# Performance work log

Hardware: AMD Instinct MI355X
Metric: run time of the kernel (lower is better)

Reference implementation:

```python
import jax, jax.numpy as jnp
import numpy as np

E = 20    # number of residue types (rc.restypes)
NB = 2    # num_blocks per AngleHead
NA = 7    # num_angles
C_S = 384
C_H = 128
BS, L = 8, 2048


def setup_inputs() -> dict:
    key = jax.random.key(0)
    ks = jax.random.split(key, 16)
    sc = 0.02
    return {
        "s": jax.random.normal(ks[0], (BS, L, C_S), dtype=jnp.float32),
        "s_init": jax.random.normal(ks[1], (BS, L, C_S), dtype=jnp.float32),
        "aatype": jax.random.randint(ks[2], (BS, L), 0, E, dtype=jnp.int32),
        # stacked per-residue-type AngleHead params
        "Win": jax.random.normal(ks[3], (E, C_S, C_H), dtype=jnp.float32) * sc,
        "b_in": jax.random.normal(ks[4], (E, C_H), dtype=jnp.float32) * sc,
        "Winit": jax.random.normal(ks[5], (E, C_S, C_H), dtype=jnp.float32) * sc,
        "b_init2": jax.random.normal(ks[6], (E, C_H), dtype=jnp.float32) * sc,
        "Wb1": jax.random.normal(ks[7], (E, NB, C_H, C_H), dtype=jnp.float32) * sc,
        "bb1": jax.random.normal(ks[8], (E, NB, C_H), dtype=jnp.float32) * sc,
        "Wb2": jax.random.normal(ks[9], (E, NB, C_H, C_H), dtype=jnp.float32) * sc,
        "bb2": jax.random.normal(ks[10], (E, NB, C_H), dtype=jnp.float32) * sc,
        "Wout": jax.random.normal(ks[11], (E, C_H, NA * 2), dtype=jnp.float32) * sc,
        "b_out": jax.random.normal(ks[12], (E, NA * 2), dtype=jnp.float32) * sc,
    }


def reference(s, s_init, aatype, Win, b_in, Winit, b_init2, Wb1, bb1, Wb2, bb2, Wout, b_out):
    relu = jax.nn.relu
    bs, seq_len, c_s = s.shape
    N = bs * seq_len
    sf = s.reshape(N, c_s)          # [N, c_s]
    si = s_init.reshape(N, c_s)     # [N, c_s]

    # Dense dispatch: run every token through all E per-type heads, then
    # combine with the one-hot routing mask (math identical to the torch
    # gather/scatter loop over residue types).
    h = jnp.einsum('nd,edh->neh', relu(sf), Win) + b_in            # [N,E,H]
    h = h + jnp.einsum('nd,edh->neh', relu(si), Winit) + b_init2   # [N,E,H]

    for b in range(NB):  # ResidualBlock1d: s + W2 @ relu(W1 @ relu(s))
        a = jnp.einsum('neh,ehk->nek', relu(h), Wb1[:, b]) + bb1[:, b]
        a = jnp.einsum('nek,ekh->neh', relu(a), Wb2[:, b]) + bb2[:, b]
        h = h + a

    out = jnp.einsum('neh,eho->neo', relu(h), Wout) + b_out        # [N,E,2*NA]
    sel = jax.nn.one_hot(aatype.reshape(N), E, dtype=out.dtype)    # [N,E]
    ang = jnp.einsum('neo,ne->no', out, sel).reshape(bs, seq_len, NA, 2)

    # F.normalize(dim=-1): x / max(||x||, eps)
    nrm = jnp.maximum(jnp.linalg.norm(ang, axis=-1, keepdims=True), 1e-12)
    return ang / nrm
```

## Files before the change

### kernel.cpp

```cpp
#include <hip/hip_runtime.h>
#include <math.h>

#define E_TYPES 20
#define NBLK 2
#define NANG 7
#define CS 384
#define CH 128
#define N_TOK (8 * 2048)
#define TOK 32
#define TPB 256
#define KC 128
#define MAX_TILES (N_TOK / TOK + E_TYPES)
#define PADN 2048

#define CNT_OFF 0
#define PERM_OFF 64
#define WT1_OFF (256 * 1024)
#define WT1_SZ  (20 * 8 * 24 * 2048)
#define WTR_OFF (WT1_OFF + WT1_SZ)

typedef __attribute__((ext_vector_type(8))) short bfrag;
typedef __attribute__((ext_vector_type(4))) float f32x4;

__device__ __forceinline__ void split_bf16(float x, unsigned short& h, unsigned short& l) {
    unsigned int u = __float_as_uint(x);
    unsigned int hb = (u + 0x7FFFu + ((u >> 16) & 1u)) & 0xFFFF0000u;
    h = (unsigned short)(hb >> 16);
    float r = x - __uint_as_float(hb);
    unsigned int v = __float_as_uint(r);
    l = (unsigned short)((v + 0x7FFFu + ((v >> 16) & 1u)) >> 16);
}

__global__ __launch_bounds__(TPB)
void prep_k(const float* __restrict__ Win, const float* __restrict__ Winit,
            const float* __restrict__ Wb1, const float* __restrict__ Wb2,
            const int* __restrict__ aatype, int* __restrict__ wsI,
            unsigned short* __restrict__ wt)
{
    __shared__ unsigned short tp[4][2][32][134];
    __shared__ int lh[E_TYPES], lcur[E_TYPES];
    int bid = blockIdx.x, t = threadIdx.x;

    if (bid < 64) {
        if (t < E_TYPES) { lh[t] = 0; lcur[t] = 0; }
        __syncthreads();
        for (int i = t; i < bid * 256; i += 256) atomicAdd(&lh[aatype[i]], 1);
        __syncthreads();
        int idx = bid * 256 + t;
        int e = aatype[idx];
        int r = lh[e] + atomicAdd(&lcur[e], 1);
        if (r < PADN) wsI[PERM_OFF + e * PADN + r] = idx;
        if (bid == 63) {
            __syncthreads();
            if (t < E_TYPES) wsI[CNT_OFF + t] = lh[t] + lcur[t];
        }
        return;
    }

    int w = t >> 6, lane = t & 63, lane15 = lane & 15, quad = lane >> 4;
    int wid = (bid - 64) * 4 + w;
    const float* srcbase;
    int phase1, e, kt, m4 = 0;
    if (wid < 480) {
        phase1 = 1;
        e = wid / 24; kt = wid % 24;
        srcbase = (kt < 12) ? Win   + ((size_t)e * CS + kt * 32) * CH
                            : Winit + ((size_t)e * CS + (kt - 12) * 32) * CH;
    } else {
        phase1 = 0;
        int rid = wid - 480;
        e = rid >> 4; m4 = (rid >> 2) & 3; kt = rid & 3;
        const float* W = (m4 & 1) ? Wb2 : Wb1;
        srcbase = W + (((size_t)e * NBLK + (m4 >> 1)) * CH + kt * 32) * CH;
    }

    #pragma unroll 4
    for (int i = 0; i < 16; i++) {
        int idx = i * 64 + lane;
        int row = idx >> 5, c4 = idx & 31;
        float4 v = *(const float4*)(srcbase + (size_t)row * CH + c4 * 4);
        ushort4 hv, lv;
        split_bf16(v.x, hv.x, lv.x);
        split_bf16(v.y, hv.y, lv.y);
        split_bf16(v.z, hv.z, lv.z);
        split_bf16(v.w, hv.w, lv.w);
        *(ushort4*)&tp[w][0][row][c4 * 4] = hv;
        *(ushort4*)&tp[w][1][row][c4 * 4] = lv;
    }
    #pragma unroll
    for (int nt = 0; nt < 8; nt++) {
        bfrag hb, lb;
        #pragma unroll
        for (int j = 0; j < 8; j++) {
            hb[j] = (short)tp[w][0][quad * 8 + j][nt * 16 + lane15];
            lb[j] = (short)tp[w][1][quad * 8 + j][nt * 16 + lane15];
        }
        size_t blk = phase1 ? (size_t)((e * 8 + nt) * 24 + kt)
                            : (size_t)((((e * 4 + m4) * 8) + nt) * 4 + kt);
        unsigned short* dst = wt + (phase1 ? WT1_OFF / 2 : WTR_OFF / 2)
                              + blk * 1024 + lane * 8;
        *(bfrag*)dst = hb;
        *(bfrag*)(dst + 512) = lb;
    }
}

#define MFMA(a, b, c) __builtin_amdgcn_mfma_f32_16x16x32_bf16((a), (b), (c), 0, 0, 0)

__global__ __launch_bounds__(TPB)
void angle_main(const float* __restrict__ s, const float* __restrict__ si,
                const float* __restrict__ b_in, const float* __restrict__ b_init2,
                const float* __restrict__ bb1, const float* __restrict__ bb2,
                const float* __restrict__ Wout, const float* __restrict__ b_out,
                const int* __restrict__ wsI, const unsigned short* __restrict__ wt,
                float* __restrict__ out)
{
    __shared__ __align__(16) unsigned short Afrag[2][2][512][8];
    __shared__ float Hf[TOK][132];
    __shared__ float Of[TOK][16];
    __shared__ int ptok[TOK];
    __shared__ int poffs[E_TYPES + 1];

    int t = threadIdx.x;
    if (t == 0) {
        int off = 0;
        for (int e = 0; e < E_TYPES; e++) {
            poffs[e] = off;
            off += (wsI[CNT_OFF + e] + TOK - 1) & ~(TOK - 1);
        }
        poffs[E_TYPES] = off;
    }
    __syncthreads();

    int pos = blockIdx.x * TOK;
    if (pos >= poffs[E_TYPES]) return;
    int e = 0;
    while (e < E_TYPES - 1 && pos >= poffs[e + 1]) e++;
    int n = wsI[CNT_OFF + e] - (pos - poffs[e]);
    if (n > TOK) n = TOK;
    if (t < TOK)
        ptok[t] = wsI[PERM_OFF + e * PADN + (pos - poffs[e]) + ((t < n) ? t : 0)];
    __syncthreads();

    int w = t >> 6, lane = t & 63, lane15 = lane & 15, quad = lane >> 4;
    int nc0 = (2 * w) * 16 + lane15, nc1 = nc0 + 16;

    const bfrag* wt1 = (const bfrag*)((const char*)wt + WT1_OFF);
    const bfrag* wtr = (const bfrag*)((const char*)wt + WTR_OFF);

    f32x4 acc[2][2];
    {
        float bv0 = b_in[e * CH + nc0] + b_init2[e * CH + nc0];
        float bv1 = b_in[e * CH + nc1] + b_init2[e * CH + nc1];
        #pragma unroll
        for (int mt = 0; mt < 2; mt++) {
            acc[mt][0] = (f32x4){bv0, bv0, bv0, bv0};
            acc[mt][1] = (f32x4){bv1, bv1, bv1, bv1};
        }
    }

    int stok = t >> 3, sc = t & 7;
    const float* rowp_s  = s  + (size_t)ptok[stok] * CS;
    const float* rowp_si = si + (size_t)ptok[stok] * CS;

    float4 pf[2][4];
    #pragma unroll
    for (int q = 0; q < 4; q++)
        pf[0][q] = *(const float4*)(rowp_s + sc * 4 + 32 * q);

    #pragma unroll
    for (int c = 0; c < 6; c++) {
        int buf = c & 1;
        __syncthreads();
        #pragma unroll
        for (int q = 0; q < 4; q++) {
            float4 v = pf[buf][q];
            ushort4 hv, lv;
            split_bf16(fmaxf(v.x, 0.f), hv.x, lv.x);
            split_bf16(fmaxf(v.y, 0.f), hv.y, lv.y);
            split_bf16(fmaxf(v.z, 0.f), hv.z, lv.z);
            split_bf16(fmaxf(v.w, 0.f), hv.w, lv.w);
            int fi = (q * 4 + (sc >> 1)) * 32 + stok;
            *(ushort4*)&Afrag[buf][0][fi][(sc & 1) * 4] = hv;
            *(ushort4*)&Afrag[buf][1][fi][(sc & 1) * 4] = lv;
        }
        if (c + 1 < 6) {
            const float* rp = ((c + 1) < 3 ? rowp_s : rowp_si) + ((c + 1) % 3) * KC;
            #pragma unroll
            for (int q = 0; q < 4; q++)
                pf[(c + 1) & 1][q] = *(const float4*)(rp + sc * 4 + 32 * q);
        }
        __syncthreads();
        #pragma unroll
        for (int ks = 0; ks < 4; ks++) {
            int kb = c * 4 + ks;
            int fib = (ks * 4 + quad) * 32;
            bfrag ah0 = *(const bfrag*)&Afrag[buf][0][fib + lane15][0];
            bfrag ah1 = *(const bfrag*)&Afrag[buf][0][fib + 16 + lane15][0];
            bfrag al0 = *(const bfrag*)&Afrag[buf][1][fib + lane15][0];
            bfrag al1 = *(const bfrag*)&Afrag[buf][1][fib + 16 + lane15][0];
            size_t b0 = ((size_t)(e * 8 + 2 * w) * 24 + kb) * 128;
            size_t b1 = ((size_t)(e * 8 + 2 * w + 1) * 24 + kb) * 128;
            bfrag bh0 = wt1[b0 + lane], bl0 = wt1[b0 + 64 + lane];
            bfrag bh1 = wt1[b1 + lane], bl1 = wt1[b1 + 64 + lane];
            acc[0][0] = MFMA(ah0, bh0, acc[0][0]);
            acc[0][0] = MFMA(ah0, bl0, acc[0][0]);
            acc[0][0] = MFMA(al0, bh0, acc[0][0]);
            acc[0][1] = MFMA(ah0, bh1, acc[0][1]);
            acc[0][1] = MFMA(ah0, bl1, acc[0][1]);
            acc[0][1] = MFMA(al0, bh1, acc[0][1]);
            acc[1][0] = MFMA(ah1, bh0, acc[1][0]);
            acc[1][0] = MFMA(ah1, bl0, acc[1][0]);
            acc[1][0] = MFMA(al1, bh0, acc[1][0]);
            acc[1][1] = MFMA(ah1, bh1, acc[1][1]);
            acc[1][1] = MFMA(ah1, bl1, acc[1][1]);
            acc[1][1] = MFMA(al1, bh1, acc[1][1]);
        }
    }

    #pragma unroll
    for (int b = 0; b < NBLK; b++) {
        f32x4 a2[2][2];
        #pragma unroll
        for (int stage = 0; stage < 2; stage++) {
            int g = 2 * b + stage;
            __syncthreads();
            #pragma unroll
            for (int mt = 0; mt < 2; mt++)
                #pragma unroll
                for (int nl = 0; nl < 2; nl++) {
                    f32x4 v = (stage == 0) ? acc[mt][nl] : a2[mt][nl];
                    int nn = (2 * w + nl) * 16 + lane15;
                    int fib = ((nn >> 5) * 4 + ((nn >> 3) & 3)) * 32;
                    int j = nn & 7;
                    #pragma unroll
                    for (int r = 0; r < 4; r++) {
                        int m = mt * 16 + quad * 4 + r;
                        unsigned short hh, ll;
                        split_bf16(fmaxf(v[r], 0.f), hh, ll);
                        Afrag[0][0][fib + m][j] = hh;
                        Afrag[0][1][fib + m][j] = ll;
                    }
                }
            __syncthreads();

            const float* bias = (stage == 0) ? bb1 : bb2;
            f32x4 an[2][2];
            {
                float bv0 = bias[(e * NBLK + b) * CH + nc0];
                float bv1 = bias[(e * NBLK + b) * CH + nc1];
                #pragma unroll
                for (int mt = 0; mt < 2; mt++) {
                    an[mt][0] = (f32x4){bv0, bv0, bv0, bv0};
                    an[mt][1] = (f32x4){bv1, bv1, bv1, bv1};
                }
            }
            #pragma unroll
            for (int ks = 0; ks < 4; ks++) {
                int fib = (ks * 4 + quad) * 32;
                bfrag ah0 = *(const bfrag*)&Afrag[0][0][fib + lane15][0];
                bfrag ah1 = *(const bfrag*)&Afrag[0][0][fib + 16 + lane15][0];
                bfrag al0 = *(const bfrag*)&Afrag[0][1][fib + lane15][0];
                bfrag al1 = *(const bfrag*)&Afrag[0][1][fib + 16 + lane15][0];
                size_t b0 = ((size_t)((e * 4 + g) * 8 + 2 * w) * 4 + ks) * 128;
                size_t b1 = ((size_t)((e * 4 + g) * 8 + 2 * w + 1) * 4 + ks) * 128;
                bfrag bh0 = wtr[b0 + lane], bl0 = wtr[b0 + 64 + lane];
                bfrag bh1 = wtr[b1 + lane], bl1 = wtr[b1 + 64 + lane];
                an[0][0] = MFMA(ah0, bh0, an[0][0]);
                an[0][0] = MFMA(ah0, bl0, an[0][0]);
                an[0][0] = MFMA(al0, bh0, an[0][0]);
                an[0][1] = MFMA(ah0, bh1, an[0][1]);
                an[0][1] = MFMA(ah0, bl1, an[0][1]);
                an[0][1] = MFMA(al0, bh1, an[0][1]);
                an[1][0] = MFMA(ah1, bh0, an[1][0]);
                an[1][0] = MFMA(ah1, bl0, an[1][0]);
                an[1][0] = MFMA(al1, bh0, an[1][0]);
                an[1][1] = MFMA(ah1, bh1, an[1][1]);
                an[1][1] = MFMA(ah1, bl1, an[1][1]);
                an[1][1] = MFMA(al1, bh1, an[1][1]);
            }
            if (stage == 0) {
                #pragma unroll
                for (int mt = 0; mt < 2; mt++)
                    #pragma unroll
                    for (int nl = 0; nl < 2; nl++) a2[mt][nl] = an[mt][nl];
            } else {
                #pragma unroll
                for (int mt = 0; mt < 2; mt++)
                    #pragma unroll
                    for (int nl = 0; nl < 2; nl++) acc[mt][nl] += an[mt][nl];
            }
        }
    }

    __syncthreads();
    #pragma unroll
    for (int mt = 0; mt < 2; mt++)
        #pragma unroll
        for (int nl = 0; nl < 2; nl++) {
            f32x4 v = acc[mt][nl];
            int nn = (2 * w + nl) * 16 + lane15;
            #pragma unroll
            for (int r = 0; r < 4; r++)
                Hf[mt * 16 + quad * 4 + r][nn] = fmaxf(v[r], 0.f);
        }
    __syncthreads();

    const float* WoutE = Wout + (size_t)e * CH * (NANG * 2);
    const float* boutE = b_out + (size_t)e * (NANG * 2);
    for (int idx = t; idx < n * (NANG * 2); idx += TPB) {
        int i = idx / (NANG * 2);
        int o = idx % (NANG * 2);
        float v = boutE[o];
        #pragma unroll 4
        for (int k = 0; k < CH; k++)
            v = fmaf(Hf[i][k], WoutE[(size_t)k * (NANG * 2) + o], v);
        Of[i][o] = v;
    }
    __syncthreads();

    for (int idx = t; idx < n * NANG; idx += TPB) {
        int i = idx / NANG;
        int a = idx % NANG;
        float x = Of[i][2 * a];
        float y = Of[i][2 * a + 1];
        float nr = fmaxf(sqrtf(x * x + y * y), 1e-12f);
        size_t base = (size_t)ptok[i] * (NANG * 2) + 2 * a;
        out[base]     = x / nr;
        out[base + 1] = y / nr;
    }
}

extern "C" void kernel_launch(void* const* d_in, const int* in_sizes, int n_in,
                              void* d_out, int out_size, void* d_ws, size_t ws_size,
                              hipStream_t stream) {
    const float* s       = (const float*)d_in[0];
    const float* s_init  = (const float*)d_in[1];
    const int*   aatype  = (const int*)d_in[2];
    const float* Win     = (const float*)d_in[3];
    const float* b_in    = (const float*)d_in[4];
    const float* Winit   = (const float*)d_in[5];
    const float* b_init2 = (const float*)d_in[6];
    const float* Wb1     = (const float*)d_in[7];
    const float* bb1     = (const float*)d_in[8];
    const float* Wb2     = (const float*)d_in[9];
    const float* bb2     = (const float*)d_in[10];
    const float* Wout    = (const float*)d_in[11];
    const float* b_out   = (const float*)d_in[12];
    int* wsI = (int*)d_ws;
    unsigned short* wt = (unsigned short*)d_ws;
    float* out = (float*)d_out;

    hipLaunchKernelGGL(prep_k, dim3(64 + 200), dim3(TPB), 0, stream,
                       Win, Winit, Wb1, Wb2, aatype, wsI, wt);
    hipLaunchKernelGGL(angle_main, dim3(MAX_TILES), dim3(TPB), 0, stream,
                       s, s_init, b_in, b_init2, bb1, bb2, Wout, b_out,
                       wsI, wt, out);
}
```

Before: 164.8 us.

## Split token tile across 8 waves, alias shared memory, remap block order

```diff
diff --git a/kernel.cpp b/kernel.cpp
--- a/kernel.cpp
+++ b/kernel.cpp
@@ -8,9 +8,10 @@
 #define CH 128
 #define N_TOK (8 * 2048)
 #define TOK 32
-#define TPB 256
-#define KC 128
+#define TPB 512
+#define PREPB 256
 #define MAX_TILES (N_TOK / TOK + E_TYPES)
+#define GRID_M 536
 #define PADN 2048
 
 #define CNT_OFF 0
@@ -31,7 +32,7 @@
     l = (unsigned short)((v + 0x7FFFu + ((v >> 16) & 1u)) >> 16);
 }
 
-__global__ __launch_bounds__(TPB)
+__global__ __launch_bounds__(PREPB)
 void prep_k(const float* __restrict__ Win, const float* __restrict__ Winit,
             const float* __restrict__ Wb1, const float* __restrict__ Wb2,
             const int* __restrict__ aatype, int* __restrict__ wsI,
@@ -114,9 +115,11 @@
                 const int* __restrict__ wsI, const unsigned short* __restrict__ wt,
                 float* __restrict__ out)
 {
-    __shared__ __align__(16) unsigned short Afrag[2][2][512][8];
-    __shared__ float Hf[TOK][132];
-    __shared__ float Of[TOK][16];
+    __shared__ __align__(16) unsigned char smem_raw[32768];
+    typedef unsigned short AfragT[2][2][512][8];
+    AfragT& Afrag = *reinterpret_cast<AfragT*>(smem_raw);
+    float (*Hf)[130] = reinterpret_cast<float(*)[130]>(smem_raw);
+    float (*Of)[16]  = reinterpret_cast<float(*)[16]>(smem_raw + 16640);
     __shared__ int ptok[TOK];
     __shared__ int poffs[E_TYPES + 1];
 
@@ -131,7 +134,9 @@
     }
     __syncthreads();
 
-    int pos = blockIdx.x * TOK;
+    int bid = blockIdx.x;
+    int tile = (bid & 7) * (GRID_M / 8) + (bid >> 3);
+    int pos = tile * TOK;
     if (pos >= poffs[E_TYPES]) return;
     int e = 0;
     while (e < E_TYPES - 1 && pos >= poffs[e + 1]) e++;
@@ -139,170 +144,141 @@
     if (n > TOK) n = TOK;
     if (t < TOK)
         ptok[t] = wsI[PERM_OFF + e * PADN + (pos - poffs[e]) + ((t < n) ? t : 0)];
-    __syncthreads();
 
     int w = t >> 6, lane = t & 63, lane15 = lane & 15, quad = lane >> 4;
-    int nc0 = (2 * w) * 16 + lane15, nc1 = nc0 + 16;
+    int mw = w >> 2;
+    int np = w & 3;
+    int nc0 = (2 * np) * 16 + lane15, nc1 = nc0 + 16;
+
+    __syncthreads();
 
     const bfrag* wt1 = (const bfrag*)((const char*)wt + WT1_OFF);
     const bfrag* wtr = (const bfrag*)((const char*)wt + WTR_OFF);
 
-    f32x4 acc[2][2];
+    f32x4 acc[2];
     {
         float bv0 = b_in[e * CH + nc0] + b_init2[e * CH + nc0];
         float bv1 = b_in[e * CH + nc1] + b_init2[e * CH + nc1];
-        #pragma unroll
-        for (int mt = 0; mt < 2; mt++) {
-            acc[mt][0] = (f32x4){bv0, bv0, bv0, bv0};
-            acc[mt][1] = (f32x4){bv1, bv1, bv1, bv1};
-        }
-    }
-
-    int stok = t >> 3, sc = t & 7;
+        acc[0] = (f32x4){bv0, bv0, bv0, bv0};
+        acc[1] = (f32x4){bv1, bv1, bv1, bv1};
+    }
+
+    int stok = t >> 4, sc = t & 15;
     const float* rowp_s  = s  + (size_t)ptok[stok] * CS;
     const float* rowp_si = si + (size_t)ptok[stok] * CS;
 
-    float4 pf[2][4];
-    #pragma unroll
-    for (int q = 0; q < 4; q++)
-        pf[0][q] = *(const float4*)(rowp_s + sc * 4 + 32 * q);
+    float4 pf[2][2];
+    #pragma unroll
+    for (int q = 0; q < 2; q++)
+        pf[0][q] = *(const float4*)(rowp_s + sc * 4 + 64 * q);
 
     #pragma unroll
     for (int c = 0; c < 6; c++) {
         int buf = c & 1;
         __syncthreads();
         #pragma unroll
-        for (int q = 0; q < 4; q++) {
+        for (int q = 0; q < 2; q++) {
             float4 v = pf[buf][q];
             ushort4 hv, lv;
             split_bf16(fmaxf(v.x, 0.f), hv.x, lv.x);
             split_bf16(fmaxf(v.y, 0.f), hv.y, lv.y);
             split_bf16(fmaxf(v.z, 0.f), hv.z, lv.z);
             split_bf16(fmaxf(v.w, 0.f), hv.w, lv.w);
-            int fi = (q * 4 + (sc >> 1)) * 32 + stok;
+            int fi = ((sc >> 1) + 8 * q) * 32 + stok;
             *(ushort4*)&Afrag[buf][0][fi][(sc & 1) * 4] = hv;
             *(ushort4*)&Afrag[buf][1][fi][(sc & 1) * 4] = lv;
         }
         if (c + 1 < 6) {
-            const float* rp = ((c + 1) < 3 ? rowp_s : rowp_si) + ((c + 1) % 3) * KC;
+            const float* rp = ((c + 1) < 3 ? rowp_s : rowp_si) + ((c + 1) % 3) * 128;
             #pragma unroll
-            for (int q = 0; q < 4; q++)
-                pf[(c + 1) & 1][q] = *(const float4*)(rp + sc * 4 + 32 * q);
+            for (int q = 0; q < 2; q++)
+                pf[(c + 1) & 1][q] = *(const float4*)(rp + sc * 4 + 64 * q);
         }
         __syncthreads();
         #pragma unroll
         for (int ks = 0; ks < 4; ks++) {
             int kb = c * 4 + ks;
-            int fib = (ks * 4 + quad) * 32;
-            bfrag ah0 = *(const bfrag*)&Afrag[buf][0][fib + lane15][0];
-            bfrag ah1 = *(const bfrag*)&Afrag[buf][0][fib + 16 + lane15][0];
-            bfrag al0 = *(const bfrag*)&Afrag[buf][1][fib + lane15][0];
-            bfrag al1 = *(const bfrag*)&Afrag[buf][1][fib + 16 + lane15][0];
-            size_t b0 = ((size_t)(e * 8 + 2 * w) * 24 + kb) * 128;
-            size_t b1 = ((size_t)(e * 8 + 2 * w + 1) * 24 + kb) * 128;
+            int fib = (ks * 4 + quad) * 32 + mw * 16;
+            bfrag ah = *(const bfrag*)&Afrag[buf][0][fib + lane15][0];
+            bfrag al = *(const bfrag*)&Afrag[buf][1][fib + lane15][0];
+            size_t b0 = ((size_t)(e * 8 + 2 * np) * 24 + kb) * 128;
+            size_t b1 = ((size_t)(e * 8 + 2 * np + 1) * 24 + kb) * 128;
             bfrag bh0 = wt1[b0 + lane], bl0 = wt1[b0 + 64 + lane];
             bfrag bh1 = wt1[b1 + lane], bl1 = wt1[b1 + 64 + lane];
-            acc[0][0] = MFMA(ah0, bh0, acc[0][0]);
-            acc[0][0] = MFMA(ah0, bl0, acc[0][0]);
-            acc[0][0] = MFMA(al0, bh0, acc[0][0]);
-            acc[0][1] = MFMA(ah0, bh1, acc[0][1]);
-            acc[0][1] = MFMA(ah0, bl1, acc[0][1]);
-            acc[0][1] = MFMA(al0, bh1, acc[0][1]);
-            acc[1][0] = MFMA(ah1, bh0, acc[1][0]);
-            acc[1][0] = MFMA(ah1, bl0, acc[1][0]);
-            acc[1][0] = MFMA(al1, bh0, acc[1][0]);
-            acc[1][1] = MFMA(ah1, bh1, acc[1][1]);
-            acc[1][1] = MFMA(ah1, bl1, acc[1][1]);
-            acc[1][1] = MFMA(al1, bh1, acc[1][1]);
-        }
-    }
-
+            acc[0] = MFMA(ah, bh0, acc[0]);
+            acc[0] = MFMA(ah, bl0, acc[0]);
+            acc[0] = MFMA(al, bh0, acc[0]);
+            acc[1] = MFMA(ah, bh1, acc[1]);
+            acc[1] = MFMA(ah, bl1, acc[1]);
+            acc[1] = MFMA(al, bh1, acc[1]);
+        }
+    }
+
+    f32x4 a2[2];
     #pragma unroll
     for (int b = 0; b < NBLK; b++) {
-        f32x4 a2[2][2];
         #pragma unroll
         for (int stage = 0; stage < 2; stage++) {
             int g = 2 * b + stage;
             __syncthreads();
             #pragma unroll
-            for (int mt = 0; mt < 2; mt++)
+            for (int nl = 0; nl < 2; nl++) {
+                f32x4 v = (stage == 0) ? acc[nl] : a2[nl];
+                int nn = (2 * np + nl) * 16 + lane15;
+                int fib = ((nn >> 5) * 4 + ((nn >> 3) & 3)) * 32;
+                int j = nn & 7;
                 #pragma unroll
-                for (int nl = 0; nl < 2; nl++) {
-                    f32x4 v = (stage == 0) ? acc[mt][nl] : a2[mt][nl];
-                    int nn = (2 * w + nl) * 16 + lane15;
-                    int fib = ((nn >> 5) * 4 + ((nn >> 3) & 3)) * 32;
-                    int j = nn & 7;
-                    #pragma unroll
-                    for (int r = 0; r < 4; r++) {
-                        int m = mt * 16 + quad * 4 + r;
-                        unsigned short hh, ll;
-                        split_bf16(fmaxf(v[r], 0.f), hh, ll);
-                        Afrag[0][0][fib + m][j] = hh;
-                        Afrag[0][1][fib + m][j] = ll;
-                    }
+                for (int r = 0; r < 4; r++) {
+                    int m = mw * 16 + quad * 4 + r;
+                    unsigned short hh, ll;
+                    split_bf16(fmaxf(v[r], 0.f), hh, ll);
+                    Afrag[0][0][fib + m][j] = hh;
+                    Afrag[0][1][fib + m][j] = ll;
                 }
+            }
             __syncthreads();
 
             const float* bias = (stage == 0) ? bb1 : bb2;
-            f32x4 an[2][2];
+            f32x4 an[2];
             {
                 float bv0 = bias[(e * NBLK + b) * CH + nc0];
                 float bv1 = bias[(e * NBLK + b) * CH + nc1];
-                #pragma unroll
-                for (int mt = 0; mt < 2; mt++) {
-                    an[mt][0] = (f32x4){bv0, bv0, bv0, bv0};
-                    an[mt][1] = (f32x4){bv1, bv1, bv1, bv1};
-                }
+                an[0] = (f32x4){bv0, bv0, bv0, bv0};
+                an[1] = (f32x4){bv1, bv1, bv1, bv1};
             }
             #pragma unroll
             for (int ks = 0; ks < 4; ks++) {
-                int fib = (ks * 4 + quad) * 32;
-                bfrag ah0 = *(const bfrag*)&Afrag[0][0][fib + lane15][0];
-                bfrag ah1 = *(const bfrag*)&Afrag[0][0][fib + 16 + lane15][0];
-                bfrag al0 = *(const bfrag*)&Afrag[0][1][fib + lane15][0];
-                bfrag al1 = *(const bfrag*)&Afrag[0][1][fib + 16 + lane15][0];
-                size_t b0 = ((size_t)((e * 4 + g) * 8 + 2 * w) * 4 + ks) * 128;
-                size_t b1 = ((size_t)((e * 4 + g) * 8 + 2 * w + 1) * 4 + ks) * 128;
+                int fib = (ks * 4 + quad) * 32 + mw * 16;
+                bfrag ah = *(const bfrag*)&Afrag[0][0][fib + lane15][0];
+                bfrag al = *(const bfrag*)&Afrag[0][1][fib + lane15][0];
+                size_t b0 = ((size_t)((e * 4 + g) * 8 + 2 * np) * 4 + ks) * 128;
+                size_t b1 = ((size_t)((e * 4 + g) * 8 + 2 * np + 1) * 4 + ks) * 128;
                 bfrag bh0 = wtr[b0 + lane], bl0 = wtr[b0 + 64 + lane];
                 bfrag bh1 = wtr[b1 + lane], bl1 = wtr[b1 + 64 + lane];
-                an[0][0] = MFMA(ah0, bh0, an[0][0]);
-                an[0][0] = MFMA(ah0, bl0, an[0][0]);
-                an[0][0] = MFMA(al0, bh0, an[0][0]);
-                an[0][1] = MFMA(ah0, bh1, an[0][1]);
-                an[0][1] = MFMA(ah0, bl1, an[0][1]);
-                an[0][1] = MFMA(al0, bh1, an[0][1]);
-                an[1][0] = MFMA(ah1, bh0, an[1][0]);
-                an[1][0] = MFMA(ah1, bl0, an[1][0]);
-                an[1][0] = MFMA(al1, bh0, an[1][0]);
-                an[1][1] = MFMA(ah1, bh1, an[1][1]);
-                an[1][1] = MFMA(ah1, bl1, an[1][1]);
-                an[1][1] = MFMA(al1, bh1, an[1][1]);
+                an[0] = MFMA(ah, bh0, an[0]);
+                an[0] = MFMA(ah, bl0, an[0]);
+                an[0] = MFMA(al, bh0, an[0]);
+                an[1] = MFMA(ah, bh1, an[1]);
+                an[1] = MFMA(ah, bl1, an[1]);
+                an[1] = MFMA(al, bh1, an[1]);
             }
             if (stage == 0) {
-                #pragma unroll
-                for (int mt = 0; mt < 2; mt++)
-                    #pragma unroll
-                    for (int nl = 0; nl < 2; nl++) a2[mt][nl] = an[mt][nl];
+                a2[0] = an[0]; a2[1] = an[1];
             } else {
-                #pragma unroll
-                for (int mt = 0; mt < 2; mt++)
-                    #pragma unroll
-                    for (int nl = 0; nl < 2; nl++) acc[mt][nl] += an[mt][nl];
+                acc[0] += an[0]; acc[1] += an[1];
             }
         }
     }
 
     __syncthreads();
     #pragma unroll
-    for (int mt = 0; mt < 2; mt++)
-        #pragma unroll
-        for (int nl = 0; nl < 2; nl++) {
-            f32x4 v = acc[mt][nl];
-            int nn = (2 * w + nl) * 16 + lane15;
-            #pragma unroll
-            for (int r = 0; r < 4; r++)
-                Hf[mt * 16 + quad * 4 + r][nn] = fmaxf(v[r], 0.f);
-        }
+    for (int nl = 0; nl < 2; nl++) {
+        f32x4 v = acc[nl];
+        int nn = (2 * np + nl) * 16 + lane15;
+        #pragma unroll
+        for (int r = 0; r < 4; r++)
+            Hf[mw * 16 + quad * 4 + r][nn] = fmaxf(v[r], 0.f);
+    }
     __syncthreads();
 
     const float* WoutE = Wout + (size_t)e * CH * (NANG * 2);
@@ -350,9 +326,9 @@
     unsigned short* wt = (unsigned short*)d_ws;
     float* out = (float*)d_out;
 
-    hipLaunchKernelGGL(prep_k, dim3(64 + 200), dim3(TPB), 0, stream,
+    hipLaunchKernelGGL(prep_k, dim3(64 + 200), dim3(PREPB), 0, stream,
                        Win, Winit, Wb1, Wb2, aatype, wsI, wt);
-    hipLaunchKernelGGL(angle_main, dim3(MAX_TILES), dim3(TPB), 0, stream,
+    hipLaunchKernelGGL(angle_main, dim3(GRID_M), dim3(TPB), 0, stream,
                        s, s_init, b_in, b_init2, bb1, bb2, Wout, b_out,
                        wsI, wt, out);
 }
```

New measurement: 174.9 us. 6.1% more time.

## Prefetch B weight fragments, alias LDS buffers, and swizzle tile order

Applied to the files above, without the earlier changes.

```diff
diff --git a/kernel.cpp b/kernel.cpp
--- a/kernel.cpp
+++ b/kernel.cpp
@@ -9,8 +9,8 @@
 #define N_TOK (8 * 2048)
 #define TOK 32
 #define TPB 256
-#define KC 128
-#define MAX_TILES (N_TOK / TOK + E_TYPES)
+#define PREPB 256
+#define GRID_M 536
 #define PADN 2048
 
 #define CNT_OFF 0
@@ -31,7 +31,7 @@
     l = (unsigned short)((v + 0x7FFFu + ((v >> 16) & 1u)) >> 16);
 }
 
-__global__ __launch_bounds__(TPB)
+__global__ __launch_bounds__(PREPB)
 void prep_k(const float* __restrict__ Win, const float* __restrict__ Winit,
             const float* __restrict__ Wb1, const float* __restrict__ Wb2,
             const int* __restrict__ aatype, int* __restrict__ wsI,
@@ -106,6 +106,20 @@
 
 #define MFMA(a, b, c) __builtin_amdgcn_mfma_f32_16x16x32_bf16((a), (b), (c), 0, 0, 0)
 
+#define KSTEP(AH0, AL0, AH1, AL1, B, ACC)                    \
+    ACC[0][0] = MFMA(AH0, B[0], ACC[0][0]);                  \
+    ACC[0][0] = MFMA(AH0, B[1], ACC[0][0]);                  \
+    ACC[0][0] = MFMA(AL0, B[0], ACC[0][0]);                  \
+    ACC[0][1] = MFMA(AH0, B[2], ACC[0][1]);                  \
+    ACC[0][1] = MFMA(AH0, B[3], ACC[0][1]);                  \
+    ACC[0][1] = MFMA(AL0, B[2], ACC[0][1]);                  \
+    ACC[1][0] = MFMA(AH1, B[0], ACC[1][0]);                  \
+    ACC[1][0] = MFMA(AH1, B[1], ACC[1][0]);                  \
+    ACC[1][0] = MFMA(AL1, B[0], ACC[1][0]);                  \
+    ACC[1][1] = MFMA(AH1, B[2], ACC[1][1]);                  \
+    ACC[1][1] = MFMA(AH1, B[3], ACC[1][1]);                  \
+    ACC[1][1] = MFMA(AL1, B[2], ACC[1][1]);
+
 __global__ __launch_bounds__(TPB)
 void angle_main(const float* __restrict__ s, const float* __restrict__ si,
                 const float* __restrict__ b_in, const float* __restrict__ b_init2,
@@ -114,24 +128,26 @@
                 const int* __restrict__ wsI, const unsigned short* __restrict__ wt,
                 float* __restrict__ out)
 {
-    __shared__ __align__(16) unsigned short Afrag[2][2][512][8];
-    __shared__ float Hf[TOK][132];
-    __shared__ float Of[TOK][16];
+    __shared__ __align__(16) unsigned char smem_raw[32768];
+    typedef unsigned short AfragT[2][2][512][8];
+    AfragT& Afrag = *reinterpret_cast<AfragT*>(smem_raw);
+    float (*Hf)[132] = reinterpret_cast<float(*)[132]>(smem_raw);
+    float (*Of)[16]  = reinterpret_cast<float(*)[16]>(smem_raw + 16896);
     __shared__ int ptok[TOK];
     __shared__ int poffs[E_TYPES + 1];
 
     int t = threadIdx.x;
-    if (t == 0) {
+    if (t <= E_TYPES) {
         int off = 0;
-        for (int e = 0; e < E_TYPES; e++) {
-            poffs[e] = off;
+        for (int e = 0; e < t; e++)
             off += (wsI[CNT_OFF + e] + TOK - 1) & ~(TOK - 1);
-        }
-        poffs[E_TYPES] = off;
-    }
-    __syncthreads();
-
-    int pos = blockIdx.x * TOK;
+        poffs[t] = off;
+    }
+    __syncthreads();
+
+    int bid = blockIdx.x;
+    int tile = (bid & 7) * (GRID_M / 8) + (bid >> 3);
+    int pos = tile * TOK;
     if (pos >= poffs[E_TYPES]) return;
     int e = 0;
     while (e < E_TYPES - 1 && pos >= poffs[e + 1]) e++;
@@ -139,10 +155,11 @@
     if (n > TOK) n = TOK;
     if (t < TOK)
         ptok[t] = wsI[PERM_OFF + e * PADN + (pos - poffs[e]) + ((t < n) ? t : 0)];
-    __syncthreads();
 
     int w = t >> 6, lane = t & 63, lane15 = lane & 15, quad = lane >> 4;
     int nc0 = (2 * w) * 16 + lane15, nc1 = nc0 + 16;
+
+    __syncthreads();
 
     const bfrag* wt1 = (const bfrag*)((const char*)wt + WT1_OFF);
     const bfrag* wtr = (const bfrag*)((const char*)wt + WTR_OFF);
@@ -166,6 +183,8 @@
     #pragma unroll
     for (int q = 0; q < 4; q++)
         pf[0][q] = *(const float4*)(rowp_s + sc * 4 + 32 * q);
+
+    bfrag Bc[4], Bn[4];
 
     #pragma unroll
     for (int c = 0; c < 6; c++) {
@@ -183,43 +202,42 @@
             *(ushort4*)&Afrag[buf][0][fi][(sc & 1) * 4] = hv;
             *(ushort4*)&Afrag[buf][1][fi][(sc & 1) * 4] = lv;
         }
+        __syncthreads();
         if (c + 1 < 6) {
-            const float* rp = ((c + 1) < 3 ? rowp_s : rowp_si) + ((c + 1) % 3) * KC;
+            const float* rp = ((c + 1) < 3 ? rowp_s : rowp_si) + ((c + 1) % 3) * 128;
             #pragma unroll
             for (int q = 0; q < 4; q++)
                 pf[(c + 1) & 1][q] = *(const float4*)(rp + sc * 4 + 32 * q);
         }
-        __syncthreads();
+        {
+            size_t b0 = ((size_t)(e * 8 + 2 * w) * 24 + c * 4) * 128;
+            size_t b1 = ((size_t)(e * 8 + 2 * w + 1) * 24 + c * 4) * 128;
+            Bc[0] = wt1[b0 + lane]; Bc[1] = wt1[b0 + 64 + lane];
+            Bc[2] = wt1[b1 + lane]; Bc[3] = wt1[b1 + 64 + lane];
+        }
         #pragma unroll
         for (int ks = 0; ks < 4; ks++) {
-            int kb = c * 4 + ks;
+            if (ks < 3) {
+                int kb = c * 4 + ks + 1;
+                size_t b0 = ((size_t)(e * 8 + 2 * w) * 24 + kb) * 128;
+                size_t b1 = ((size_t)(e * 8 + 2 * w + 1) * 24 + kb) * 128;
+                Bn[0] = wt1[b0 + lane]; Bn[1] = wt1[b0 + 64 + lane];
+                Bn[2] = wt1[b1 + lane]; Bn[3] = wt1[b1 + 64 + lane];
+            }
             int fib = (ks * 4 + quad) * 32;
             bfrag ah0 = *(const bfrag*)&Afrag[buf][0][fib + lane15][0];
             bfrag ah1 = *(const bfrag*)&Afrag[buf][0][fib + 16 + lane15][0];
             bfrag al0 = *(const bfrag*)&Afrag[buf][1][fib + lane15][0];
             bfrag al1 = *(const bfrag*)&Afrag[buf][1][fib + 16 + lane15][0];
-            size_t b0 = ((size_t)(e * 8 + 2 * w) * 24 + kb) * 128;
-            size_t b1 = ((size_t)(e * 8 + 2 * w + 1) * 24 + kb) * 128;
-            bfrag bh0 = wt1[b0 + lane], bl0 = wt1[b0 + 64 + lane];
-            bfrag bh1 = wt1[b1 + lane], bl1 = wt1[b1 + 64 + lane];
-            acc[0][0] = MFMA(ah0, bh0, acc[0][0]);
-            acc[0][0] = MFMA(ah0, bl0, acc[0][0]);
-            acc[0][0] = MFMA(al0, bh0, acc[0][0]);
-            acc[0][1] = MFMA(ah0, bh1, acc[0][1]);
-            acc[0][1] = MFMA(ah0, bl1, acc[0][1]);
-            acc[0][1] = MFMA(al0, bh1, acc[0][1]);
-            acc[1][0] = MFMA(ah1, bh0, acc[1][0]);
-            acc[1][0] = MFMA(ah1, bl0, acc[1][0]);
-            acc[1][0] = MFMA(al1, bh0, acc[1][0]);
-            acc[1][1] = MFMA(ah1, bh1, acc[1][1]);
-            acc[1][1] = MFMA(ah1, bl1, acc[1][1]);
-            acc[1][1] = MFMA(al1, bh1, acc[1][1]);
-        }
-    }
-
+            KSTEP(ah0, al0, ah1, al1, Bc, acc)
+            #pragma unroll
+            for (int z = 0; z < 4; z++) Bc[z] = Bn[z];
+        }
+    }
+
+    f32x4 a2[2][2];
     #pragma unroll
     for (int b = 0; b < NBLK; b++) {
-        f32x4 a2[2][2];
         #pragma unroll
         for (int stage = 0; stage < 2; stage++) {
             int g = 2 * b + stage;
@@ -254,29 +272,28 @@
                     an[mt][1] = (f32x4){bv1, bv1, bv1, bv1};
                 }
             }
+            {
+                size_t b0 = ((size_t)((e * 4 + g) * 8 + 2 * w) * 4) * 128;
+                size_t b1 = ((size_t)((e * 4 + g) * 8 + 2 * w + 1) * 4) * 128;
+                Bc[0] = wtr[b0 + lane]; Bc[1] = wtr[b0 + 64 + lane];
+                Bc[2] = wtr[b1 + lane]; Bc[3] = wtr[b1 + 64 + lane];
+            }
             #pragma unroll
             for (int ks = 0; ks < 4; ks++) {
+                if (ks < 3) {
+                    size_t b0 = ((size_t)((e * 4 + g) * 8 + 2 * w) * 4 + ks + 1) * 128;
+                    size_t b1 = ((size_t)((e * 4 + g) * 8 + 2 * w + 1) * 4 + ks + 1) * 128;
+                    Bn[0] = wtr[b0 + lane]; Bn[1] = wtr[b0 + 64 + lane];
+                    Bn[2] = wtr[b1 + lane]; Bn[3] = wtr[b1 + 64 + lane];
+                }
                 int fib = (ks * 4 + quad) * 32;
                 bfrag ah0 = *(const bfrag*)&Afrag[0][0][fib + lane15][0];
                 bfrag ah1 = *(const bfrag*)&Afrag[0][0][fib + 16 + lane15][0];
                 bfrag al0 = *(const bfrag*)&Afrag[0][1][fib + lane15][0];
                 bfrag al1 = *(const bfrag*)&Afrag[0][1][fib + 16 + lane15][0];
-                size_t b0 = ((size_t)((e * 4 + g) * 8 + 2 * w) * 4 + ks) * 128;
-                size_t b1 = ((size_t)((e * 4 + g) * 8 + 2 * w + 1) * 4 + ks) * 128;
-                bfrag bh0 = wtr[b0 + lane], bl0 = wtr[b0 + 64 + lane];
-                bfrag bh1 = wtr[b1 + lane], bl1 = wtr[b1 + 64 + lane];
-                an[0][0] = MFMA(ah0, bh0, an[0][0]);
-                an[0][0] = MFMA(ah0, bl0, an[0][0]);
-                an[0][0] = MFMA(al0, bh0, an[0][0]);
-                an[0][1] = MFMA(ah0, bh1, an[0][1]);
-                an[0][1] = MFMA(ah0, bl1, an[0][1]);
-                an[0][1] = MFMA(al0, bh1, an[0][1]);
-                an[1][0] = MFMA(ah1, bh0, an[1][0]);
-                an[1][0] = MFMA(ah1, bl0, an[1][0]);
-                an[1][0] = MFMA(al1, bh0, an[1][0]);
-                an[1][1] = MFMA(ah1, bh1, an[1][1]);
-                an[1][1] = MFMA(ah1, bl1, an[1][1]);
-                an[1][1] = MFMA(al1, bh1, an[1][1]);
+                KSTEP(ah0, al0, ah1, al1, Bc, an)
+                #pragma unroll
+                for (int z = 0; z < 4; z++) Bc[z] = Bn[z];
             }
             if (stage == 0) {
                 #pragma unroll
@@ -350,9 +367,9 @@
     unsigned short* wt = (unsigned short*)d_ws;
     float* out = (float*)d_out;
 
-    hipLaunchKernelGGL(prep_k, dim3(64 + 200), dim3(TPB), 0, stream,
+    hipLaunchKernelGGL(prep_k, dim3(64 + 200), dim3(PREPB), 0, stream,
                        Win, Winit, Wb1, Wb2, aatype, wsI, wt);
-    hipLaunchKernelGGL(angle_main, dim3(MAX_TILES), dim3(TPB), 0, stream,
+    hipLaunchKernelGGL(angle_main, dim3(GRID_M), dim3(TPB), 0, stream,
                        s, s_init, b_in, b_init2, bb1, bb2, Wout, b_out,
                        wsI, wt, out);
 }
```

After: 168.2 us. 1.02x slower.
